# Optimization experiments

Measured on AMD Instinct MI355X. Metric: run time of the kernel, lower is better.

## Reference

```python
import jax, jax.numpy as jnp
import numpy as np

N, E, DIN, H = 10000, 80000, 1024, 512
NEG = 0.2  # PyG GATv2Conv default negative_slope


def gatv2(x, src, dst, wl, bl, wr, br, att, b, n):
    # GATv2: e_ij = att . leaky_relu(Wl x_j + Wr x_i); segment softmax over dst; sum alpha * Wl x_j
    xl = x @ wl + bl            # [N, H] source transform
    xr = x @ wr + br            # [N, H] target transform
    z = jax.nn.leaky_relu(xl[src] + xr[dst], NEG)   # [E, H]
    e = z @ att                                      # [E]
    m = jax.ops.segment_max(e, dst, num_segments=n)  # per-target max (self-loops guarantee nonempty)
    p = jnp.exp(e - m[dst])
    s = jax.ops.segment_sum(p, dst, num_segments=n)
    alpha = p / (s[dst] + 1e-16)                     # [E]
    out = jax.ops.segment_sum(alpha[:, None] * xl[src], dst, num_segments=n)
    return out + b


def setup_inputs() -> dict:
    key = jax.random.key(0)
    ks = iter(jax.random.split(key, 64))
    d = {}
    d["x"] = jax.random.normal(next(ks), (N, DIN), jnp.float32)
    d["edge_index"] = jax.random.randint(next(ks), (2, E), 0, N, dtype=jnp.int32).astype(jnp.int64)
    dims = [DIN, H, H, H]
    for i in range(4):
        din = dims[i]
        sc = 1.0 / np.sqrt(din)
        d[f"wl{i+1}"] = jax.random.normal(next(ks), (din, H), jnp.float32) * sc
        d[f"bl{i+1}"] = jnp.zeros((H,), jnp.float32)
        d[f"wr{i+1}"] = jax.random.normal(next(ks), (din, H), jnp.float32) * sc
        d[f"br{i+1}"] = jnp.zeros((H,), jnp.float32)
        d[f"att{i+1}"] = jax.random.normal(next(ks), (H,), jnp.float32) * (1.0 / np.sqrt(H))
        d[f"b{i+1}"] = jnp.zeros((H,), jnp.float32)
    for name, din, dout in [("1", H, 512), ("2", 512, 256), ("3", 256, 2)]:
        d[f"lw{name}"] = jax.random.normal(next(ks), (din, dout), jnp.float32) * (1.0 / np.sqrt(din))
        d[f"lb{name}"] = jnp.zeros((dout,), jnp.float32)
    return d


def reference(x, edge_index, wl1, bl1, wr1, br1, att1, b1,
              wl2, bl2, wr2, br2, att2, b2,
              wl3, bl3, wr3, br3, att3, b3,
              wl4, bl4, wr4, br4, att4, b4,
              lw1, lb1, lw2, lb2, lw3, lb3):
    n = x.shape[0]
    loops = jnp.arange(n, dtype=edge_index.dtype)
    src = jnp.concatenate([edge_index[0], loops])  # add self-loops (PyG default)
    dst = jnp.concatenate([edge_index[1], loops])
    h = jax.nn.relu(gatv2(x, src, dst, wl1, bl1, wr1, br1, att1, b1, n))
    h = jax.nn.relu(gatv2(h, src, dst, wl2, bl2, wr2, br2, att2, b2, n))
    h = jax.nn.relu(gatv2(h, src, dst, wl3, bl3, wr3, br3, att3, b3, n))
    h = jax.nn.relu(gatv2(h, src, dst, wl4, bl4, wr4, br4, att4, b4, n))
    # dropout is identity at inference
    h = jax.nn.relu(h @ lw1 + lb1)
    h = jax.nn.relu(h @ lw2 + lb2)
    logits = h @ lw3 + lb3
    return logits, jax.nn.softmax(logits, axis=1)
```

## Files before the change

kernel.cpp:

```cpp
#include <hip/hip_runtime.h>
#include <cstdint>

#define NN 10000
#define NE 80000
#define DIN_ 1024
#define HH 512

typedef __attribute__((ext_vector_type(8))) short bf16x8;
typedef __attribute__((ext_vector_type(4))) float f32x4;
typedef unsigned short u16;
typedef unsigned int u32;

static __device__ __forceinline__ float b2f(u16 u) {
  u32 i = ((u32)u) << 16;
  return __builtin_bit_cast(float, i);
}
static __device__ __forceinline__ u16 f2b(float f) {
  u32 i = __builtin_bit_cast(u32, f);
  u32 r = (i + 0x7fffu + ((i >> 16) & 1u)) >> 16;
  return (u16)r;
}
static __device__ __forceinline__ void unpack8(uint4 u, float* f) {
  f[0] = __builtin_bit_cast(float, u.x << 16);
  f[1] = __builtin_bit_cast(float, u.x & 0xffff0000u);
  f[2] = __builtin_bit_cast(float, u.y << 16);
  f[3] = __builtin_bit_cast(float, u.y & 0xffff0000u);
  f[4] = __builtin_bit_cast(float, u.z << 16);
  f[5] = __builtin_bit_cast(float, u.z & 0xffff0000u);
  f[6] = __builtin_bit_cast(float, u.w << 16);
  f[7] = __builtin_bit_cast(float, u.w & 0xffff0000u);
}
static __device__ __forceinline__ void load8(const u16* p, float* f) { unpack8(*(const uint4*)p, f); }

#define ASYNC_CP16(gp, lp)                                                        \
  __builtin_amdgcn_global_load_lds((__attribute__((address_space(1))) void*)(gp), \
                                   (__attribute__((address_space(3))) void*)(lp), \
                                   16, 0, 0)

static __device__ __forceinline__ int float_flag(const u16* xw) {
  __shared__ int c;
  if (threadIdx.x == 0) c = 0;
  __syncthreads();
  int bad = 0;
  for (int i = threadIdx.x; i < 2048; i += blockDim.x) {
    u32 e = (xw[i] >> 7) & 0xFFu;
    if (e >= 140u) bad++;
  }
  if (bad) atomicAdd(&c, bad);
  __syncthreads();
  return c > 64;
}
static __device__ __forceinline__ int int64_flag(const u32* ew) {
  __shared__ int c;
  if (threadIdx.x == 0) c = 0;
  __syncthreads();
  int z = 0;
  for (int i = threadIdx.x; i < 256; i += blockDim.x)
    if (ew[2 * i + 1] == 0u) z++;
  if (z) atomicAdd(&c, z);
  __syncthreads();
  return c > 200;
}

__global__ void k_edges(const void* ei, int* esrc, int* edst, int* counts) {
  int f64 = int64_flag((const u32*)ei);
  int i = blockIdx.x * 256 + threadIdx.x;
  if (i < NE) {
    int sv, dv;
    if (f64) {
      sv = (int)((const long long*)ei)[i];
      dv = (int)((const long long*)ei)[NE + i];
    } else {
      sv = ((const int*)ei)[i];
      dv = ((const int*)ei)[NE + i];
    }
    esrc[i] = sv;
    edst[i] = dv;
    atomicAdd(&counts[dv], 1);
  } else if (i < NE + NN) {
    atomicAdd(&counts[i - NE], 1);
  }
}

#define CONVB 2047
__global__ __launch_bounds__(512) void k_scanconv(const int* counts, int* rowptr, int* cursor, int n,
                                                  const void* xin, u16* xout) {
  if (blockIdx.x == 0) {
    __shared__ int lds[512];
    const int PER = 20;
    int t = threadIdx.x;
    int base = t * PER;
    int v[PER];
    int sum = 0;
#pragma unroll
    for (int i = 0; i < PER; i++) {
      int idx = base + i;
      v[i] = (idx < n) ? counts[idx] : 0;
      sum += v[i];
    }
    lds[t] = sum;
    __syncthreads();
    for (int off = 1; off < 512; off <<= 1) {
      int x = (t >= off) ? lds[t - off] : 0;
      __syncthreads();
      lds[t] += x;
      __syncthreads();
    }
    int run = (t > 0) ? lds[t - 1] : 0;
#pragma unroll
    for (int i = 0; i < PER; i++) {
      int idx = base + i;
      if (idx < n) {
        cursor[idx] = run;
        run += v[i];
        rowptr[idx + 1] = run;
      }
    }
    if (t == 0) rowptr[0] = 0;
    return;
  }
  int f = float_flag((const u16*)xin);
  const int total = NN * DIN_ / 8;
  for (int g = (blockIdx.x - 1) * 512 + threadIdx.x; g < total; g += CONVB * 512) {
    u16 o[8];
    if (f) {
      const float* p = (const float*)xin + (size_t)g * 8;
#pragma unroll
      for (int i = 0; i < 8; i++) o[i] = f2b(p[i]);
    } else {
      *(uint4*)o = *((const uint4*)xin + g);
    }
    *((uint4*)xout + g) = *(const uint4*)o;
  }
}

#define SBLK 352
struct Prep {
  const int* esrc;
  const int* edst;
  int* cursor;
  int* col;
  const void* xin;
  const void* vin[20];
  u16* vout[20];
  int vn[20];
  const void* tin[10];
  u16* tout[10];
  int tK[10], tN[10], toff[10];
};
__global__ void k_prep(Prep a) {
  __shared__ u16 tt[32][33];
  int b = blockIdx.x;
  if (b < SBLK) {
    int i = b * 256 + threadIdx.x;
    if (i < NE) {
      int p = atomicAdd(&a.cursor[a.edst[i]], 1);
      a.col[p] = a.esrc[i];
    } else if (i < NE + NN) {
      int v = i - NE;
      int p = atomicAdd(&a.cursor[v], 1);
      a.col[p] = v;
    }
    return;
  }
  b -= SBLK;
  int f = float_flag((const u16*)a.xin);
  if (b < 20) {
    int v = b;
    const void* in = a.vin[v];
    u16* out = a.vout[v];
    int n = a.vn[v];
    for (int i = threadIdx.x; i < n; i += 256)
      out[i] = f ? f2b(((const float*)in)[i]) : ((const u16*)in)[i];
  } else {
    int tb = b - 20;
    int seg = 0;
#pragma unroll
    for (int i = 1; i < 10; i++)
      if (tb >= a.toff[i]) seg = i;
    int tl = tb - a.toff[seg];
    int K = a.tK[seg], N = a.tN[seg];
    int tiles_n = N >> 5;
    int n0 = (tl % tiles_n) << 5, k0 = (tl / tiles_n) << 5;
    const void* in = a.tin[seg];
    u16* out = a.tout[seg];
    int tx = threadIdx.x & 31, ty = threadIdx.x >> 5;
    for (int r = ty; r < 32; r += 8) {
      size_t idx = (size_t)(k0 + r) * N + n0 + tx;
      tt[r][tx] = f ? f2b(((const float*)in)[idx]) : ((const u16*)in)[idx];
    }
    __syncthreads();
    for (int r = ty; r < 32; r += 8) out[(size_t)(n0 + r) * K + k0 + tx] = tt[tx][r];
  }
}

__global__ __launch_bounds__(256) void k_gemm64(const u16* __restrict__ A, int lda,
                                                const u16* __restrict__ Bt,
                                                const u16* __restrict__ bias,
                                                u16* __restrict__ C,
                                                int M, int N, int K, int act,
                                                int tiles_m, int ln_tiles_n) {
  __shared__ u16 sA[2 * 64 * 32];
  __shared__ u16 sB[2 * 128 * 32];
  int id = blockIdx.x;
  int xcd = id & 7;
  int rest = id >> 3;
  int xt = rest & ((1 << ln_tiles_n) - 1);
  int yt = ((rest >> ln_tiles_n) << 3) + xcd;
  if (yt >= tiles_m) return;
  int m0 = yt << 6, n0 = xt << 7;
  int t = threadIdx.x;
  int wave = t >> 6, lane = t & 63;

  int srow = t >> 2;
  int sk = ((t & 3) ^ ((t >> 3) & 3)) * 8;
  const u16* agp[2];
  u16* la[2];
#pragma unroll
  for (int h = 0; h < 2; h++) {
    int ra = m0 + srow;
    ra = ra < M ? ra : M - 1;
    agp[h] = A + (size_t)ra * lda + h * 32 + sk;
    la[h] = sA + h * 2048 + t * 8;
  }
  const u16* bgp[4];
  u16* lb[4];
#pragma unroll
  for (int q = 0; q < 4; q++) {
    int h = q >> 1;
    int row = ((q & 1) << 6) + srow;
    bgp[q] = Bt + (size_t)(n0 + row) * K + h * 32 + sk;
    lb[q] = sB + h * 4096 + (((q & 1) << 8) + t) * 8;
  }

  int wn = wave << 5;
  int lr = lane & 15;
  int kcs = (((lane >> 4) ^ ((lr >> 1) & 3))) * 8;

  f32x4 acc[4][2];
#pragma unroll
  for (int i = 0; i < 4; i++)
#pragma unroll
    for (int j = 0; j < 2; j++) acc[i][j] = (f32x4){0.f, 0.f, 0.f, 0.f};

  for (int k0 = 0; k0 < K; k0 += 64) {
#pragma unroll
    for (int h = 0; h < 2; h++) ASYNC_CP16(agp[h] + k0, la[h]);
#pragma unroll
    for (int q = 0; q < 4; q++) ASYNC_CP16(bgp[q] + k0, lb[q]);
    __syncthreads();
    bf16x8 a[2][4], b[2][2];
#pragma unroll
    for (int s = 0; s < 2; s++) {
#pragma unroll
      for (int i = 0; i < 4; i++) a[s][i] = *(const bf16x8*)(sA + s * 2048 + (i * 16 + lr) * 32 + kcs);
#pragma unroll
      for (int j = 0; j < 2; j++) b[s][j] = *(const bf16x8*)(sB + s * 4096 + (wn + j * 16 + lr) * 32 + kcs);
    }
#pragma unroll
    for (int s = 0; s < 2; s++)
#pragma unroll
      for (int i = 0; i < 4; i++)
#pragma unroll
        for (int j = 0; j < 2; j++)
          acc[i][j] = __builtin_amdgcn_mfma_f32_16x16x32_bf16(a[s][i], b[s][j], acc[i][j], 0, 0, 0);
    __syncthreads();
  }

  int rbase = (lane >> 4) << 2;
#pragma unroll
  for (int j = 0; j < 2; j++) {
    int colc = n0 + wn + j * 16 + lr;
    float bv = b2f(bias[colc]);
#pragma unroll
    for (int i = 0; i < 4; i++) {
#pragma unroll
      for (int r = 0; r < 4; r++) {
        int row = m0 + i * 16 + rbase + r;
        if (row < M) {
          float v = acc[i][j][r] + bv;
          if (act) v = fmaxf(v, 0.f);
          C[(size_t)row * N + colc] = f2b(v);
        }
      }
    }
  }
}

__global__ __launch_bounds__(256) void k_attn5(u16* __restrict__ xlr,
                                               const u16* __restrict__ att, const u16* __restrict__ bias,
                                               const int* __restrict__ rowptr, const int* __restrict__ col,
                                               int n) {
  int node = (blockIdx.x * 256 + threadIdx.x) >> 6;
  if (node >= n) return;
  int lane = threadIdx.x & 63;
  int h0 = lane * 8;
  float a[8], r[8];
  load8(att + h0, a);
  load8(xlr + (size_t)node * 1024 + 512 + h0, r);
  int e0 = rowptr[node], e1 = rowptr[node + 1];

  float m = -3e38f, s = 0.f;
  float acc[8] = {0.f, 0.f, 0.f, 0.f, 0.f, 0.f, 0.f, 0.f};
  int j0 = col[e0];
  int j1 = col[(e0 + 1 < e1) ? e0 + 1 : e0];
  uint4 raw0 = *(const uint4*)(xlr + (size_t)j0 * 1024 + h0);
  uint4 raw1 = *(const uint4*)(xlr + (size_t)j1 * 1024 + h0);

  for (int e = e0; e < e1; e += 2) {
    bool has2 = (e + 1 < e1);
    int jn0 = col[(e + 2 < e1) ? e + 2 : e1 - 1];
    int jn1 = col[(e + 3 < e1) ? e + 3 : e1 - 1];
    uint4 p0 = *(const uint4*)(xlr + (size_t)jn0 * 1024 + h0);
    uint4 p1 = *(const uint4*)(xlr + (size_t)jn1 * 1024 + h0);
    float x0[8], x1[8];
    unpack8(raw0, x0);
    unpack8(raw1, x1);
    float pa = 0.f, pb = 0.f;
#pragma unroll
    for (int i = 0; i < 8; i++) {
      float z0 = x0[i] + r[i];
      z0 = z0 > 0.f ? z0 : 0.2f * z0;
      pa = fmaf(a[i], z0, pa);
      float z1 = x1[i] + r[i];
      z1 = z1 > 0.f ? z1 : 0.2f * z1;
      pb = fmaf(a[i], z1, pb);
    }
#pragma unroll
    for (int off = 32; off >= 1; off >>= 1) {
      pa += __shfl_xor(pa, off);
      pb += __shfl_xor(pb, off);
    }
    if (pa > m) {
      float al = __expf(m - pa);
      s = fmaf(s, al, 1.f);
#pragma unroll
      for (int i = 0; i < 8; i++) acc[i] = fmaf(acc[i], al, x0[i]);
      m = pa;
    } else {
      float w = __expf(pa - m);
      s += w;
#pragma unroll
      for (int i = 0; i < 8; i++) acc[i] = fmaf(w, x0[i], acc[i]);
    }
    if (has2) {
      if (pb > m) {
        float al = __expf(m - pb);
        s = fmaf(s, al, 1.f);
#pragma unroll
        for (int i = 0; i < 8; i++) acc[i] = fmaf(acc[i], al, x1[i]);
        m = pb;
      } else {
        float w = __expf(pb - m);
        s += w;
#pragma unroll
        for (int i = 0; i < 8; i++) acc[i] = fmaf(w, x1[i], acc[i]);
      }
    }
    raw0 = p0;
    raw1 = p1;
  }
  float inv = 1.f / (s + 1e-16f);

  float bv[8];
  load8(bias + h0, bv);
  uint4 o;
  u32 p8[8];
#pragma unroll
  for (int i = 0; i < 8; i++) {
    float v = fmaf(acc[i], inv, bv[i]);
    v = fmaxf(v, 0.f);
    p8[i] = f2b(v);
  }
  o.x = p8[0] | (p8[1] << 16);
  o.y = p8[2] | (p8[3] << 16);
  o.z = p8[4] | (p8[5] << 16);
  o.w = p8[6] | (p8[7] << 16);
  *(uint4*)(xlr + (size_t)node * 1024 + 512 + h0) = o;
}

__global__ __launch_bounds__(256) void k_head(const u16* __restrict__ h2, const u16* __restrict__ lw3,
                                              const u16* __restrict__ lb3, float* __restrict__ out, int n) {
  int row = (blockIdx.x * 256 + threadIdx.x) >> 6;
  if (row >= n) return;
  int lane = threadIdx.x & 63;
  int k0 = lane * 4;
  uint2 hu = *(const uint2*)(h2 + (size_t)row * 256 + k0);
  float hx[4];
  hx[0] = __builtin_bit_cast(float, hu.x << 16);
  hx[1] = __builtin_bit_cast(float, hu.x & 0xffff0000u);
  hx[2] = __builtin_bit_cast(float, hu.y << 16);
  hx[3] = __builtin_bit_cast(float, hu.y & 0xffff0000u);
  float wv[8];
  load8(lw3 + (size_t)k0 * 2, wv);
  float p0 = 0.f, p1 = 0.f;
#pragma unroll
  for (int i = 0; i < 4; i++) {
    p0 = fmaf(hx[i], wv[2 * i], p0);
    p1 = fmaf(hx[i], wv[2 * i + 1], p1);
  }
#pragma unroll
  for (int off = 32; off >= 1; off >>= 1) {
    p0 += __shfl_xor(p0, off);
    p1 += __shfl_xor(p1, off);
  }
  if (lane == 0) {
    float l0 = p0 + b2f(lb3[0]);
    float l1 = p1 + b2f(lb3[1]);
    float mx = fmaxf(l0, l1);
    float q0 = __expf(l0 - mx), q1 = __expf(l1 - mx);
    float si = 1.f / (q0 + q1);
    out[row * 2 + 0] = l0;
    out[row * 2 + 1] = l1;
    out[2 * n + row * 2 + 0] = q0 * si;
    out[2 * n + row * 2 + 1] = q1 * si;
  }
}

extern "C" void kernel_launch(void* const* d_in, const int* in_sizes, int n_in,
                              void* d_out, int out_size, void* d_ws, size_t ws_size,
                              hipStream_t stream) {
  (void)in_sizes; (void)n_in; (void)out_size; (void)ws_size;
  const void* x_raw = d_in[0];
  const void* ei_raw = d_in[1];
  const void *wl[4], *bl[4], *wr[4], *br[4], *att[4], *bg[4];
  for (int i = 0; i < 4; i++) {
    wl[i] = d_in[2 + i * 6 + 0];
    bl[i] = d_in[2 + i * 6 + 1];
    wr[i] = d_in[2 + i * 6 + 2];
    br[i] = d_in[2 + i * 6 + 3];
    att[i] = d_in[2 + i * 6 + 4];
    bg[i] = d_in[2 + i * 6 + 5];
  }
  const void* lw1 = d_in[26];
  const void* lb1 = d_in[27];
  const void* lw2 = d_in[28];
  const void* lb2 = d_in[29];
  const void* lw3 = d_in[30];
  const void* lb3 = d_in[31];

  size_t off = 0;
  auto alloc = [&](size_t bytes) -> void* {
    off = (off + 255) & ~(size_t)255;
    void* p = (char*)d_ws + off;
    off += bytes;
    return p;
  };
  int* esrc = (int*)alloc(NE * 4);
  int* edst = (int*)alloc(NE * 4);
  int* counts = (int*)alloc(NN * 4);
  int* rowptr = (int*)alloc((NN + 1) * 4);
  int* cursor = (int*)alloc(NN * 4);
  int* col = (int*)alloc((NE + NN) * 4);
  u16* cb = (u16*)alloc(4 * 1024 * 2);
  u16* attv = (u16*)alloc(4 * 512 * 2);
  u16* bgv = (u16*)alloc(4 * 512 * 2);
  u16* lb1v = (u16*)alloc(512 * 2);
  u16* lb2v = (u16*)alloc(256 * 2);
  u16* lw3v = (u16*)alloc(512 * 2);
  u16* lb3v = (u16*)alloc(2 * 2);
  u16* comb0 = (u16*)alloc((size_t)1024 * 1024 * 2);
  u16* combL[4];
  combL[0] = comb0;
  for (int l = 1; l < 4; l++) combL[l] = (u16*)alloc((size_t)1024 * 512 * 2);
  u16* lw1T = (u16*)alloc((size_t)512 * 512 * 2);
  u16* lw2T = (u16*)alloc((size_t)256 * 512 * 2);
  u16* xc = (u16*)alloc((size_t)NN * DIN_ * 2);
  u16* X0 = (u16*)alloc((size_t)NN * 1024 * 2);
  u16* X1 = (u16*)alloc((size_t)NN * 1024 * 2);
  u16* mlp1 = xc;
  u16* mlp2 = xc + (size_t)NN * 512;

  hipMemsetAsync(counts, 0, NN * 4, stream);
  int ET = NE + NN;
  k_edges<<<(ET + 255) / 256, 256, 0, stream>>>(ei_raw, esrc, edst, counts);
  k_scanconv<<<1 + CONVB, 512, 0, stream>>>(counts, rowptr, cursor, NN, x_raw, xc);

  Prep pa;
  pa.esrc = esrc;
  pa.edst = edst;
  pa.cursor = cursor;
  pa.col = col;
  pa.xin = x_raw;
  for (int l = 0; l < 4; l++) {
    pa.vin[l * 4 + 0] = bl[l];  pa.vout[l * 4 + 0] = cb + l * 1024;        pa.vn[l * 4 + 0] = 512;
    pa.vin[l * 4 + 1] = br[l];  pa.vout[l * 4 + 1] = cb + l * 1024 + 512;  pa.vn[l * 4 + 1] = 512;
    pa.vin[l * 4 + 2] = att[l]; pa.vout[l * 4 + 2] = attv + l * 512;       pa.vn[l * 4 + 2] = 512;
    pa.vin[l * 4 + 3] = bg[l];  pa.vout[l * 4 + 3] = bgv + l * 512;        pa.vn[l * 4 + 3] = 512;
  }
  pa.vin[16] = lb1; pa.vout[16] = lb1v; pa.vn[16] = 512;
  pa.vin[17] = lb2; pa.vout[17] = lb2v; pa.vn[17] = 256;
  pa.vin[18] = lw3; pa.vout[18] = lw3v; pa.vn[18] = 512;
  pa.vin[19] = lb3; pa.vout[19] = lb3v; pa.vn[19] = 2;
  const void* tin[10] = {wl[0], wr[0], wl[1], wr[1], wl[2], wr[2], wl[3], wr[3], lw1, lw2};
  u16* tout[10] = {comb0, comb0 + (size_t)512 * 1024,
                   combL[1], combL[1] + (size_t)512 * 512,
                   combL[2], combL[2] + (size_t)512 * 512,
                   combL[3], combL[3] + (size_t)512 * 512,
                   lw1T, lw2T};
  int tK[10] = {1024, 1024, 512, 512, 512, 512, 512, 512, 512, 512};
  int tN[10] = {512, 512, 512, 512, 512, 512, 512, 512, 512, 256};
  int acc_off = 0;
  for (int i = 0; i < 10; i++) {
    pa.tin[i] = tin[i];
    pa.tout[i] = tout[i];
    pa.tK[i] = tK[i];
    pa.tN[i] = tN[i];
    pa.toff[i] = acc_off;
    acc_off += (tN[i] >> 5) * (tK[i] >> 5);
  }
  k_prep<<<SBLK + 20 + acc_off, 256, 0, stream>>>(pa);

  auto gemm = [&](const u16* A, int lda, const u16* Bt, const u16* bias, u16* C,
                  int M, int Nn, int K, int act) {
    int tiles_m = (M + 63) >> 6;
    int tiles_n = Nn >> 7;
    int ln = (tiles_n == 8) ? 3 : (tiles_n == 4) ? 2 : 1;
    int mgrp = (tiles_m + 7) >> 3;
    int blocks = (mgrp << 3) * tiles_n;
    k_gemm64<<<blocks, 256, 0, stream>>>(A, lda, Bt, bias, C, M, Nn, K, act, tiles_m, ln);
  };
  auto attn = [&](u16* xlr, int l) {
    k_attn5<<<(NN * 64 + 255) / 256, 256, 0, stream>>>(xlr, attv + l * 512, bgv + l * 512,
                                                       rowptr, col, NN);
  };

  gemm(xc, 1024, comb0, cb + 0 * 1024, X0, NN, 1024, 1024, 0);
  attn(X0, 0);
  gemm(X0 + 512, 1024, combL[1], cb + 1 * 1024, X1, NN, 1024, 512, 0);
  attn(X1, 1);
  gemm(X1 + 512, 1024, combL[2], cb + 2 * 1024, X0, NN, 1024, 512, 0);
  attn(X0, 2);
  gemm(X0 + 512, 1024, combL[3], cb + 3 * 1024, X1, NN, 1024, 512, 0);
  attn(X1, 3);

  gemm(X1 + 512, 1024, lw1T, lb1v, mlp1, NN, 512, 512, 1);
  gemm(mlp1, 512, lw2T, lb2v, mlp2, NN, 256, 512, 1);
  k_head<<<(NN * 64 + 255) / 256, 256, 0, stream>>>(mlp2, lw3v, lb3v, (float*)d_out, NN);
}
```

Before: 367.8 us.

## Fuse edge histogram, scan, edge copy and x conversion into one launch

Replaces the memset, edge-conversion kernel and scan/convert kernel with a single kernel. Block 0 builds the destination histogram in LDS with shared atomics, adds self-loops implicitly, and scans it; other blocks copy edge indices and convert x. This removes two launches and the global atomic counts buffer, but serialises the 80k-edge histogram on one block, which may lengthen the critical path.

```diff
diff --git a/kernel.cpp b/kernel.cpp
--- a/kernel.cpp
+++ b/kernel.cpp
@@ -62,40 +62,35 @@
   return c > 200;
 }
 
-__global__ void k_edges(const void* ei, int* esrc, int* edst, int* counts) {
-  int f64 = int64_flag((const u32*)ei);
-  int i = blockIdx.x * 256 + threadIdx.x;
-  if (i < NE) {
-    int sv, dv;
+#define EBLK 157
+#define CONVB 2048
+__global__ __launch_bounds__(512) void k_front(const void* ei, int* esrc, int* edst,
+                                               int* rowptr, int* cursor,
+                                               const void* xin, u16* xout) {
+  __shared__ int hist[NN];
+  __shared__ int lds[512];
+  int b = blockIdx.x;
+  int t = threadIdx.x;
+  if (b == 0) {
+    for (int i = t; i < NN; i += 512) hist[i] = 0;
+    int f64 = int64_flag((const u32*)ei);
+    __syncthreads();
     if (f64) {
-      sv = (int)((const long long*)ei)[i];
-      dv = (int)((const long long*)ei)[NE + i];
+      const long long* dd = (const long long*)ei + NE;
+      for (int i = t; i < NE; i += 512) atomicAdd(&hist[(int)dd[i]], 1);
     } else {
-      sv = ((const int*)ei)[i];
-      dv = ((const int*)ei)[NE + i];
-    }
-    esrc[i] = sv;
-    edst[i] = dv;
-    atomicAdd(&counts[dv], 1);
-  } else if (i < NE + NN) {
-    atomicAdd(&counts[i - NE], 1);
-  }
-}
-
-#define CONVB 2047
-__global__ __launch_bounds__(512) void k_scanconv(const int* counts, int* rowptr, int* cursor, int n,
-                                                  const void* xin, u16* xout) {
-  if (blockIdx.x == 0) {
-    __shared__ int lds[512];
+      const int* dd = (const int*)ei + NE;
+      for (int i = t; i < NE; i += 512) atomicAdd(&hist[dd[i]], 1);
+    }
+    __syncthreads();
     const int PER = 20;
-    int t = threadIdx.x;
     int base = t * PER;
     int v[PER];
     int sum = 0;
 #pragma unroll
     for (int i = 0; i < PER; i++) {
       int idx = base + i;
-      v[i] = (idx < n) ? counts[idx] : 0;
+      v[i] = (idx < NN) ? hist[idx] + 1 : 0;
       sum += v[i];
     }
     lds[t] = sum;
@@ -110,7 +105,7 @@
 #pragma unroll
     for (int i = 0; i < PER; i++) {
       int idx = base + i;
-      if (idx < n) {
+      if (idx < NN) {
         cursor[idx] = run;
         run += v[i];
         rowptr[idx + 1] = run;
@@ -119,9 +114,23 @@
     if (t == 0) rowptr[0] = 0;
     return;
   }
+  if (b <= EBLK) {
+    int f64 = int64_flag((const u32*)ei);
+    int i = (b - 1) * 512 + t;
+    if (i < NE) {
+      if (f64) {
+        esrc[i] = (int)((const long long*)ei)[i];
+        edst[i] = (int)((const long long*)ei)[NE + i];
+      } else {
+        esrc[i] = ((const int*)ei)[i];
+        edst[i] = ((const int*)ei)[NE + i];
+      }
+    }
+    return;
+  }
   int f = float_flag((const u16*)xin);
   const int total = NN * DIN_ / 8;
-  for (int g = (blockIdx.x - 1) * 512 + threadIdx.x; g < total; g += CONVB * 512) {
+  for (int g = (b - 1 - EBLK) * 512 + t; g < total; g += CONVB * 512) {
     u16 o[8];
     if (f) {
       const float* p = (const float*)xin + (size_t)g * 8;
@@ -448,7 +457,6 @@
   };
   int* esrc = (int*)alloc(NE * 4);
   int* edst = (int*)alloc(NE * 4);
-  int* counts = (int*)alloc(NN * 4);
   int* rowptr = (int*)alloc((NN + 1) * 4);
   int* cursor = (int*)alloc(NN * 4);
   int* col = (int*)alloc((NE + NN) * 4);
@@ -471,10 +479,7 @@
   u16* mlp1 = xc;
   u16* mlp2 = xc + (size_t)NN * 512;
 
-  hipMemsetAsync(counts, 0, NN * 4, stream);
-  int ET = NE + NN;
-  k_edges<<<(ET + 255) / 256, 256, 0, stream>>>(ei_raw, esrc, edst, counts);
-  k_scanconv<<<1 + CONVB, 512, 0, stream>>>(counts, rowptr, cursor, NN, x_raw, xc);
+  k_front<<<1 + EBLK + CONVB, 512, 0, stream>>>(ei_raw, esrc, edst, rowptr, cursor, x_raw, xc);
 
   Prep pa;
   pa.esrc = esrc;
```

Result: slower. 398.6 us (+8.4%).

## Fold edge parsing into prep and fuse CSR scatter with first GEMM launch

Applied to the files above, without the earlier changes.

Edge decoding and degree counting move into the weight-prep kernel, so the separate k_edges launch goes away. The CSR column scatter now shares one launch (k_sg) with the layer-1 GEMM, using block-index partitioning, so the small scatter overlaps with GEMM tiles. Two kernel launches and their serialization gaps are removed. The GEMM blocks now carry extra LDS-free scatter blocks ahead of them, and the GEMM parameters are hardcoded.

```diff
diff --git a/kernel.cpp b/kernel.cpp
--- a/kernel.cpp
+++ b/kernel.cpp
@@ -62,84 +62,12 @@
   return c > 200;
 }
 
-__global__ void k_edges(const void* ei, int* esrc, int* edst, int* counts) {
-  int f64 = int64_flag((const u32*)ei);
-  int i = blockIdx.x * 256 + threadIdx.x;
-  if (i < NE) {
-    int sv, dv;
-    if (f64) {
-      sv = (int)((const long long*)ei)[i];
-      dv = (int)((const long long*)ei)[NE + i];
-    } else {
-      sv = ((const int*)ei)[i];
-      dv = ((const int*)ei)[NE + i];
-    }
-    esrc[i] = sv;
-    edst[i] = dv;
-    atomicAdd(&counts[dv], 1);
-  } else if (i < NE + NN) {
-    atomicAdd(&counts[i - NE], 1);
-  }
-}
-
-#define CONVB 2047
-__global__ __launch_bounds__(512) void k_scanconv(const int* counts, int* rowptr, int* cursor, int n,
-                                                  const void* xin, u16* xout) {
-  if (blockIdx.x == 0) {
-    __shared__ int lds[512];
-    const int PER = 20;
-    int t = threadIdx.x;
-    int base = t * PER;
-    int v[PER];
-    int sum = 0;
-#pragma unroll
-    for (int i = 0; i < PER; i++) {
-      int idx = base + i;
-      v[i] = (idx < n) ? counts[idx] : 0;
-      sum += v[i];
-    }
-    lds[t] = sum;
-    __syncthreads();
-    for (int off = 1; off < 512; off <<= 1) {
-      int x = (t >= off) ? lds[t - off] : 0;
-      __syncthreads();
-      lds[t] += x;
-      __syncthreads();
-    }
-    int run = (t > 0) ? lds[t - 1] : 0;
-#pragma unroll
-    for (int i = 0; i < PER; i++) {
-      int idx = base + i;
-      if (idx < n) {
-        cursor[idx] = run;
-        run += v[i];
-        rowptr[idx + 1] = run;
-      }
-    }
-    if (t == 0) rowptr[0] = 0;
-    return;
-  }
-  int f = float_flag((const u16*)xin);
-  const int total = NN * DIN_ / 8;
-  for (int g = (blockIdx.x - 1) * 512 + threadIdx.x; g < total; g += CONVB * 512) {
-    u16 o[8];
-    if (f) {
-      const float* p = (const float*)xin + (size_t)g * 8;
-#pragma unroll
-      for (int i = 0; i < 8; i++) o[i] = f2b(p[i]);
-    } else {
-      *(uint4*)o = *((const uint4*)xin + g);
-    }
-    *((uint4*)xout + g) = *(const uint4*)o;
-  }
-}
-
 #define SBLK 352
 struct Prep {
-  const int* esrc;
-  const int* edst;
-  int* cursor;
-  int* col;
+  const void* ei;
+  int* esrc;
+  int* edst;
+  int* counts;
   const void* xin;
   const void* vin[20];
   u16* vout[20];
@@ -152,14 +80,22 @@
   __shared__ u16 tt[32][33];
   int b = blockIdx.x;
   if (b < SBLK) {
+    int f64 = int64_flag((const u32*)a.ei);
     int i = b * 256 + threadIdx.x;
     if (i < NE) {
-      int p = atomicAdd(&a.cursor[a.edst[i]], 1);
-      a.col[p] = a.esrc[i];
+      int sv, dv;
+      if (f64) {
+        sv = (int)((const long long*)a.ei)[i];
+        dv = (int)((const long long*)a.ei)[NE + i];
+      } else {
+        sv = ((const int*)a.ei)[i];
+        dv = ((const int*)a.ei)[NE + i];
+      }
+      a.esrc[i] = sv;
+      a.edst[i] = dv;
+      atomicAdd(&a.counts[dv], 1);
     } else if (i < NE + NN) {
-      int v = i - NE;
-      int p = atomicAdd(&a.cursor[v], 1);
-      a.col[p] = v;
+      atomicAdd(&a.counts[i - NE], 1);
     }
     return;
   }
@@ -194,15 +130,64 @@
   }
 }
 
-__global__ __launch_bounds__(256) void k_gemm64(const u16* __restrict__ A, int lda,
-                                                const u16* __restrict__ Bt,
-                                                const u16* __restrict__ bias,
-                                                u16* __restrict__ C,
-                                                int M, int N, int K, int act,
-                                                int tiles_m, int ln_tiles_n) {
+#define CONVB 2047
+__global__ __launch_bounds__(512) void k_scanconv(const int* counts, int* rowptr, int* cursor, int n,
+                                                  const void* xin, u16* xout) {
+  if (blockIdx.x == 0) {
+    __shared__ int lds[512];
+    const int PER = 20;
+    int t = threadIdx.x;
+    int base = t * PER;
+    int v[PER];
+    int sum = 0;
+#pragma unroll
+    for (int i = 0; i < PER; i++) {
+      int idx = base + i;
+      v[i] = (idx < n) ? counts[idx] : 0;
+      sum += v[i];
+    }
+    lds[t] = sum;
+    __syncthreads();
+    for (int off = 1; off < 512; off <<= 1) {
+      int x = (t >= off) ? lds[t - off] : 0;
+      __syncthreads();
+      lds[t] += x;
+      __syncthreads();
+    }
+    int run = (t > 0) ? lds[t - 1] : 0;
+#pragma unroll
+    for (int i = 0; i < PER; i++) {
+      int idx = base + i;
+      if (idx < n) {
+        cursor[idx] = run;
+        run += v[i];
+        rowptr[idx + 1] = run;
+      }
+    }
+    if (t == 0) rowptr[0] = 0;
+    return;
+  }
+  int f = float_flag((const u16*)xin);
+  const int total = NN * DIN_ / 8;
+  for (int g = (blockIdx.x - 1) * 512 + threadIdx.x; g < total; g += CONVB * 512) {
+    u16 o[8];
+    if (f) {
+      const float* p = (const float*)xin + (size_t)g * 8;
+#pragma unroll
+      for (int i = 0; i < 8; i++) o[i] = f2b(p[i]);
+    } else {
+      *(uint4*)o = *((const uint4*)xin + g);
+    }
+    *((uint4*)xout + g) = *(const uint4*)o;
+  }
+}
+
+static __device__ __forceinline__ void gemm64_body(int id,
+    const u16* __restrict__ A, int lda, const u16* __restrict__ Bt,
+    const u16* __restrict__ bias, u16* __restrict__ C,
+    int M, int N, int K, int act, int tiles_m, int ln_tiles_n) {
   __shared__ u16 sA[2 * 64 * 32];
   __shared__ u16 sB[2 * 128 * 32];
-  int id = blockIdx.x;
   int xcd = id & 7;
   int rest = id >> 3;
   int xt = rest & ((1 << ln_tiles_n) - 1);
@@ -285,6 +270,42 @@
       }
     }
   }
+}
+
+__global__ __launch_bounds__(256) void k_gemm64(const u16* __restrict__ A, int lda,
+                                                const u16* __restrict__ Bt,
+                                                const u16* __restrict__ bias,
+                                                u16* __restrict__ C,
+                                                int M, int N, int K, int act,
+                                                int tiles_m, int ln_tiles_n) {
+  gemm64_body(blockIdx.x, A, lda, Bt, bias, C, M, N, K, act, tiles_m, ln_tiles_n);
+}
+
+struct SG {
+  const int* esrc;
+  const int* edst;
+  int* cursor;
+  int* col;
+  const u16* A;
+  const u16* Bt;
+  const u16* bias;
+  u16* C;
+};
+__global__ __launch_bounds__(256) void k_sg(SG a) {
+  int b = blockIdx.x;
+  if (b < SBLK) {
+    int i = b * 256 + threadIdx.x;
+    if (i < NE) {
+      int p = atomicAdd(&a.cursor[a.edst[i]], 1);
+      a.col[p] = a.esrc[i];
+    } else if (i < NE + NN) {
+      int v = i - NE;
+      int p = atomicAdd(&a.cursor[v], 1);
+      a.col[p] = v;
+    }
+    return;
+  }
+  gemm64_body(b - SBLK, a.A, 1024, a.Bt, a.bias, a.C, NN, 1024, 1024, 0, 157, 3);
 }
 
 __global__ __launch_bounds__(256) void k_attn5(u16* __restrict__ xlr,
@@ -472,15 +493,12 @@
   u16* mlp2 = xc + (size_t)NN * 512;
 
   hipMemsetAsync(counts, 0, NN * 4, stream);
-  int ET = NE + NN;
-  k_edges<<<(ET + 255) / 256, 256, 0, stream>>>(ei_raw, esrc, edst, counts);
-  k_scanconv<<<1 + CONVB, 512, 0, stream>>>(counts, rowptr, cursor, NN, x_raw, xc);
 
   Prep pa;
+  pa.ei = ei_raw;
   pa.esrc = esrc;
   pa.edst = edst;
-  pa.cursor = cursor;
-  pa.col = col;
+  pa.counts = counts;
   pa.xin = x_raw;
   for (int l = 0; l < 4; l++) {
     pa.vin[l * 4 + 0] = bl[l];  pa.vout[l * 4 + 0] = cb + l * 1024;        pa.vn[l * 4 + 0] = 512;
@@ -511,6 +529,19 @@
   }
   k_prep<<<SBLK + 20 + acc_off, 256, 0, stream>>>(pa);
 
+  k_scanconv<<<1 + CONVB, 512, 0, stream>>>(counts, rowptr, cursor, NN, x_raw, xc);
+
+  SG sg;
+  sg.esrc = esrc;
+  sg.edst = edst;
+  sg.cursor = cursor;
+  sg.col = col;
+  sg.A = xc;
+  sg.Bt = comb0;
+  sg.bias = cb + 0 * 1024;
+  sg.C = X0;
+  k_sg<<<SBLK + 1280, 256, 0, stream>>>(sg);
+
   auto gemm = [&](const u16* A, int lda, const u16* Bt, const u16* bias, u16* C,
                   int M, int Nn, int K, int act) {
     int tiles_m = (M + 63) >> 6;
@@ -525,7 +556,6 @@
                                                        rowptr, col, NN);
   };
 
-  gemm(xc, 1024, comb0, cb + 0 * 1024, X0, NN, 1024, 1024, 0);
   attn(X0, 0);
   gemm(X0 + 512, 1024, combL[1], cb + 1 * 1024, X1, NN, 1024, 512, 0);
   attn(X1, 1);
```

New measurement: 360.9 us. About the same (-1.9%).
